# Kernel optimization log

Hardware: AMD Instinct MI355X
Metric: run time of the kernel (lower is better)

The kernel has to match this reference:

```python
import jax, jax.numpy as jnp
import numpy as np

NUM_CAPSULE = 16
DIM_CAPSULE = 64
ROUTINGS = 3
T_EPS = 1e-07


def squash(v, axis=-1):
    # NOTE: this repo's 'squash' is v / sqrt(||v||^2 + eps) (norm-only scaling)
    s = jnp.sum(v * v, axis=axis, keepdims=True)
    return v / jnp.sqrt(s + T_EPS)


def setup_inputs() -> dict:
    key = jax.random.key(0)
    k1, k2 = jax.random.split(key)
    B, N_in, D_in = 64, 512, 1024
    x = jax.random.normal(k1, (B, N_in, D_in), dtype=jnp.float32)
    # xavier-normal-ish init for W [1, D_in, num_capsule*dim_capsule]
    fan_in, fan_out = D_in, NUM_CAPSULE * DIM_CAPSULE
    std = float(np.sqrt(2.0 / (fan_in + fan_out)))
    W = jax.random.normal(k2, (1, D_in, NUM_CAPSULE * DIM_CAPSULE), dtype=jnp.float32) * std
    return {"x": x, "W": W}


def reference(x, W):
    B, N_in, D_in = x.shape
    # u_hat: [B, N_in, num_cap*dim_cap] -> [B, num_cap, N_in, dim_cap]
    u_hat = jnp.matmul(x, W[0])
    u_hat = u_hat.reshape(B, N_in, NUM_CAPSULE, DIM_CAPSULE).transpose(0, 2, 1, 3)
    b = jnp.zeros((B, NUM_CAPSULE, N_in), dtype=u_hat.dtype)
    outputs = None
    for i in range(ROUTINGS):
        # torch code permutes to [B, N_in, num_cap], softmaxes dim=2, permutes back:
        # equivalent to softmax over the num_capsule axis (axis=1)
        c = jax.nn.softmax(b, axis=1)  # [B, num_cap, N_in]
        outputs = squash(jnp.einsum('bij,bijk->bik', c, u_hat))  # [B, num_cap, dim_cap]
        if i < ROUTINGS - 1:
            b = jnp.einsum('bik,bijk->bij', outputs, u_hat)  # [B, num_cap, N_in]
    return outputs
```

## Files before the change

kernel.cpp:

```cpp
#include <hip/hip_runtime.h>
#include <stdint.h>

#define NUM_CAP 16
#define DIM_CAP 64
#define BATCH   64
#define N_IN    512
#define D_IN    1024
#define N_COL   1024
#define M_ROWS  (BATCH*N_IN)

typedef __attribute__((ext_vector_type(8))) short short8;
typedef __attribute__((ext_vector_type(4))) float f32x4;

__device__ __forceinline__ float bf2f(unsigned int u) {
  return __uint_as_float(u << 16);
}
__device__ __forceinline__ unsigned short f2bf_rne(float f) {
  unsigned int x = __float_as_uint(f);
  x += 0x7fffu + ((x >> 16) & 1u);
  return (unsigned short)(x >> 16);
}
__device__ __forceinline__ unsigned int pack_rne(unsigned int lo, unsigned int hi) {
  const unsigned int lr = lo + (0x7fffu + ((lo >> 16) & 1u));
  const unsigned int hr = hi + (0x7fffu + ((hi >> 16) & 1u));
  return (lr >> 16) | (hr & 0xffff0000u);
}

__global__ __launch_bounds__(256) void prep(
    const float* __restrict__ x, const float* __restrict__ W,
    unsigned short* __restrict__ xb, unsigned short* __restrict__ Wt) {
  const int t = threadIdx.x;
  if (blockIdx.x < 16384) {
    const size_t i = ((size_t)blockIdx.x * 256 + t) * 8;
    const uint4 a = *(const uint4*)(x + i);
    const uint4 b = *(const uint4*)(x + i + 4);
    uint4 p;
    p.x = pack_rne(a.x, a.y); p.y = pack_rne(a.z, a.w);
    p.z = pack_rne(b.x, b.y); p.w = pack_rne(b.z, b.w);
    *(uint4*)(xb + i) = p;
  } else {
    __shared__ float tile[32][33];
    const int bid = blockIdx.x - 16384;
    const int bx = bid & 31, by = bid >> 5;
    const int tx = t & 31, ty0 = t >> 5;
    #pragma unroll
    for (int r = 0; r < 4; r++) {
      const int ty = ty0 + r * 8;
      tile[ty][tx] = W[(size_t)(by * 32 + ty) * N_COL + bx * 32 + tx];
    }
    __syncthreads();
    #pragma unroll
    for (int r = 0; r < 4; r++) {
      const int ty = ty0 + r * 8;
      Wt[(size_t)(bx * 32 + ty) * D_IN + by * 32 + tx] = f2bf_rne(tile[tx][ty]);
    }
  }
}

__global__ __launch_bounds__(256) void gemm_uhat(
    const unsigned short* __restrict__ A,
    const unsigned short* __restrict__ Bt,
    unsigned short* __restrict__ C) {
  __shared__ __align__(16) unsigned short lA[128 * 32];
  __shared__ __align__(16) unsigned short lB[128 * 32];

  const int t = threadIdx.x;
  const int wave = t >> 6, lane = t & 63;
  const int xcd = blockIdx.x & 7, local = blockIdx.x >> 3;
  const int mt = xcd * 32 + (local >> 3), nt = local & 7;
  const int m0 = mt * 128, n0 = nt * 128;
  const int wm = wave & 1, wn = wave >> 1;

  f32x4 acc[4][4] = {};

  const int srow = lane >> 2;
  const int schunk = ((lane & 3) ^ ((srow >> 1) & 3)) * 8;

  for (int kt = 0; kt < D_IN / 32; ++kt) {
    const int k0 = kt * 32;
    __syncthreads();
    #pragma unroll
    for (int s0 = 0; s0 < 2; ++s0) {
      const int s = wave + s0 * 4;
      const unsigned short* ga = A + (size_t)(m0 + s * 16 + srow) * D_IN + k0 + schunk;
      __builtin_amdgcn_global_load_lds(
          (const __attribute__((address_space(1))) void*)ga,
          (__attribute__((address_space(3))) void*)(lA + s * 512), 16, 0, 0);
      const unsigned short* gb = Bt + (size_t)(n0 + s * 16 + srow) * D_IN + k0 + schunk;
      __builtin_amdgcn_global_load_lds(
          (const __attribute__((address_space(1))) void*)gb,
          (__attribute__((address_space(3))) void*)(lB + s * 512), 16, 0, 0);
    }
    __syncthreads();

    short8 af[4], bfr[4];
    const int rsel = lane & 15;
    const int q = lane >> 4;
    const int koff = (q ^ ((rsel >> 1) & 3)) * 8;
    #pragma unroll
    for (int tm = 0; tm < 4; tm++)
      af[tm] = *(const short8*)&lA[(wm * 64 + tm * 16 + rsel) * 32 + koff];
    #pragma unroll
    for (int tn = 0; tn < 4; tn++)
      bfr[tn] = *(const short8*)&lB[(wn * 64 + tn * 16 + rsel) * 32 + koff];
    #pragma unroll
    for (int tm = 0; tm < 4; tm++)
      #pragma unroll
      for (int tn = 0; tn < 4; tn++)
        acc[tm][tn] = __builtin_amdgcn_mfma_f32_16x16x32_bf16(
            af[tm], bfr[tn], acc[tm][tn], 0, 0, 0);
  }

  const int lrow = (lane >> 4) * 4, lcol = lane & 15;
  #pragma unroll
  for (int tm = 0; tm < 4; tm++)
    #pragma unroll
    for (int tn = 0; tn < 4; tn++)
      #pragma unroll
      for (int r = 0; r < 4; r++) {
        const int row = m0 + wm * 64 + tm * 16 + lrow + r;
        const int col = n0 + wn * 64 + tn * 16 + lcol;
        C[(size_t)row * N_COL + col] = f2bf_rne(acc[tm][tn][r]);
      }
}

__global__ __launch_bounds__(256) void s1q(
    const unsigned short* __restrict__ uhat, float* __restrict__ S1q) {
  const int t = threadIdx.x;
  const int b = blockIdx.x >> 3, s = blockIdx.x & 7;
  const unsigned short* up =
      uhat + (size_t)(b * N_IN + s * 64) * N_COL + t * 4;
  float4 a = make_float4(0.f, 0.f, 0.f, 0.f);
  #pragma unroll 8
  for (int j = 0; j < 64; ++j, up += N_COL) {
    const uint2 d = *(const uint2*)up;
    a.x += bf2f(d.x & 0xffffu);
    a.y += __uint_as_float(d.x & 0xffff0000u);
    a.z += bf2f(d.y & 0xffffu);
    a.w += __uint_as_float(d.y & 0xffff0000u);
  }
  *(float4*)&S1q[(size_t)blockIdx.x * 1024 + t * 4] = a;
}

__global__ __launch_bounds__(256) void route_mid(
    const unsigned short* __restrict__ uhat,
    const float* __restrict__ Vin,
    float* __restrict__ Pout,
    const int nstrips) {
  __shared__ float sq[16 * 68];
  __shared__ float red[4][1024];
  const int t = threadIdx.x;
  const int w = t >> 6, lane = t & 63;
  const int b = blockIdx.x >> 4, jt4 = blockIdx.x & 15;
  const int jt = jt4 * 4 + w;
  const int i_l = lane >> 2, c4 = lane & 3;

  float4 v4 = make_float4(0.f, 0.f, 0.f, 0.f);
  for (int s = 0; s < nstrips; ++s) {
    const float4 ps = *(const float4*)&Vin[((size_t)b * nstrips + s) * 1024 + t * 4];
    v4.x += ps.x; v4.y += ps.y; v4.z += ps.z; v4.w += ps.w;
  }
  float ss = v4.x * v4.x + v4.y * v4.y + v4.z * v4.z + v4.w * v4.w;
  #pragma unroll
  for (int d = 1; d < 16; d <<= 1) ss += __shfl_xor(ss, d);
  const float inv = 1.f / sqrtf(ss + 1e-7f);
  const int oi = t >> 4, ok = (t & 15) * 4;
  *(float4*)&sq[oi * 68 + ok] =
      make_float4(v4.x * inv, v4.y * inv, v4.z * inv, v4.w * inv);
  __syncthreads();

  float pv[16];
  #pragma unroll
  for (int q = 0; q < 4; q++)
    *(float4*)&pv[q * 4] = *(const float4*)&sq[i_l * 68 + c4 * 16 + q * 4];

  float acc[16];
  #pragma unroll
  for (int q = 0; q < 16; q++) acc[q] = 0.f;

  const unsigned short* ub =
      uhat + (size_t)(b * N_IN + jt * 8) * N_COL + lane * 16;

  for (int jj = 0; jj < 8; ++jj, ub += N_COL) {
    const uint4 d0 = *(const uint4*)ub;
    const uint4 d1 = *(const uint4*)(ub + 8);
    float u[16];
    #define UNP(wd, o) { u[(o)] = bf2f((wd) & 0xffffu); u[(o)+1] = __uint_as_float((wd) & 0xffff0000u); }
    UNP(d0.x, 0) UNP(d0.y, 2) UNP(d0.z, 4) UNP(d0.w, 6)
    UNP(d1.x, 8) UNP(d1.y, 10) UNP(d1.z, 12) UNP(d1.w, 14)
    #undef UNP

    float dot = 0.f;
    #pragma unroll
    for (int q = 0; q < 16; q++) dot = fmaf(pv[q], u[q], dot);
    dot += __shfl_xor(dot, 1);
    dot += __shfl_xor(dot, 2);
    const float e = __expf(dot);
    float s = e;
    #pragma unroll
    for (int d = 4; d < 64; d <<= 1) s += __shfl_xor(s, d);
    const float c = e / s;
    #pragma unroll
    for (int q = 0; q < 16; q++) acc[q] = fmaf(c, u[q], acc[q]);
  }

  #pragma unroll
  for (int q = 0; q < 4; q++)
    *(float4*)&red[w][lane * 16 + q * 4] = make_float4(
        acc[q * 4 + 0], acc[q * 4 + 1], acc[q * 4 + 2], acc[q * 4 + 3]);
  __syncthreads();
  float4 s4 = make_float4(0.f, 0.f, 0.f, 0.f);
  #pragma unroll
  for (int ww = 0; ww < 4; ++ww) {
    const float4 r = *(const float4*)&red[ww][t * 4];
    s4.x += r.x; s4.y += r.y; s4.z += r.z; s4.w += r.w;
  }
  *(float4*)&Pout[(size_t)blockIdx.x * 1024 + t * 4] = s4;
}

__global__ __launch_bounds__(64) void route_last(
    const float* __restrict__ P, float* __restrict__ dst) {
  const int bi = blockIdx.x;
  const int k = threadIdx.x;
  const int b = bi >> 4, i = bi & 15;
  const float* p = P + (size_t)b * 16 * 1024 + i * 64 + k;
  float s = 0.f;
  #pragma unroll
  for (int tt = 0; tt < 16; ++tt) s += p[(size_t)tt * 1024];
  float ss = s * s;
  #pragma unroll
  for (int d = 1; d < 64; d <<= 1) ss += __shfl_xor(ss, d);
  dst[bi * 64 + k] = s / sqrtf(ss + 1e-7f);
}

extern "C" void kernel_launch(void* const* d_in, const int* in_sizes, int n_in,
                              void* d_out, int out_size, void* d_ws, size_t ws_size,
                              hipStream_t stream) {
  const float* x = (const float*)d_in[0];
  const float* W = (const float*)d_in[1];
  float* out = (float*)d_out;

  char* ws = (char*)d_ws;
  unsigned short* Wt   = (unsigned short*)ws;
  unsigned short* uhat = (unsigned short*)(ws + (size_t)(2 << 20));
  unsigned short* xb   = (unsigned short*)(ws + (size_t)66 * (1 << 20));
  float* S1 = (float*)(ws + (size_t)130 * (1 << 20));
  float* P1 = (float*)(ws + (size_t)66 * (1 << 20));
  float* P2 = (float*)(ws + (size_t)71 * (1 << 20));

  prep<<<16384 + 1024, 256, 0, stream>>>(x, W, xb, Wt);
  gemm_uhat<<<2048, 256, 0, stream>>>(xb, Wt, uhat);
  s1q<<<512, 256, 0, stream>>>(uhat, S1);
  route_mid<<<1024, 256, 0, stream>>>(uhat, S1, P1, 8);
  route_mid<<<1024, 256, 0, stream>>>(uhat, P1, P2, 16);
  route_last<<<1024, 64, 0, stream>>>(P2, out);
}
```

Measured before the change: 322.5 us.

## Fuse x bf16 conversion and first routing sum into the u_hat GEMM

Drops the separate x-to-bf16 pass: the GEMM now loads fp32 x tiles straight into LDS and truncates to bf16 while building MFMA fragments. It also computes per-tile column sums of u_hat in the GEMM epilogue, which replaces the s1q kernel that re-read all of u_hat. The aim is to avoid one full write and read of x and one extra read of u_hat. In exchange, A-tile global and LDS traffic doubles because it is fp32, rounding changes from round-to-nearest-even to truncation, the first routing sum is taken from fp32 accumulators rather than stored bf16 values, and one route_mid loop is now unrolled.

```diff
diff --git a/kernel.cpp b/kernel.cpp
--- a/kernel.cpp
+++ b/kernel.cpp
@@ -20,49 +20,37 @@
   x += 0x7fffu + ((x >> 16) & 1u);
   return (unsigned short)(x >> 16);
 }
-__device__ __forceinline__ unsigned int pack_rne(unsigned int lo, unsigned int hi) {
-  const unsigned int lr = lo + (0x7fffu + ((lo >> 16) & 1u));
-  const unsigned int hr = hi + (0x7fffu + ((hi >> 16) & 1u));
-  return (lr >> 16) | (hr & 0xffff0000u);
-}
-
-__global__ __launch_bounds__(256) void prep(
-    const float* __restrict__ x, const float* __restrict__ W,
-    unsigned short* __restrict__ xb, unsigned short* __restrict__ Wt) {
+__device__ __forceinline__ unsigned int pack_trunc(unsigned int lo, unsigned int hi) {
+  return (lo >> 16) | (hi & 0xffff0000u);
+}
+
+__global__ __launch_bounds__(256) void prep_w(
+    const float* __restrict__ W, unsigned short* __restrict__ Wt) {
+  __shared__ float tile[32][33];
   const int t = threadIdx.x;
-  if (blockIdx.x < 16384) {
-    const size_t i = ((size_t)blockIdx.x * 256 + t) * 8;
-    const uint4 a = *(const uint4*)(x + i);
-    const uint4 b = *(const uint4*)(x + i + 4);
-    uint4 p;
-    p.x = pack_rne(a.x, a.y); p.y = pack_rne(a.z, a.w);
-    p.z = pack_rne(b.x, b.y); p.w = pack_rne(b.z, b.w);
-    *(uint4*)(xb + i) = p;
-  } else {
-    __shared__ float tile[32][33];
-    const int bid = blockIdx.x - 16384;
-    const int bx = bid & 31, by = bid >> 5;
-    const int tx = t & 31, ty0 = t >> 5;
-    #pragma unroll
-    for (int r = 0; r < 4; r++) {
-      const int ty = ty0 + r * 8;
-      tile[ty][tx] = W[(size_t)(by * 32 + ty) * N_COL + bx * 32 + tx];
-    }
-    __syncthreads();
-    #pragma unroll
-    for (int r = 0; r < 4; r++) {
-      const int ty = ty0 + r * 8;
-      Wt[(size_t)(bx * 32 + ty) * D_IN + by * 32 + tx] = f2bf_rne(tile[tx][ty]);
-    }
+  const int bx = blockIdx.x & 31, by = blockIdx.x >> 5;
+  const int tx = t & 31, ty0 = t >> 5;
+  #pragma unroll
+  for (int r = 0; r < 4; r++) {
+    const int ty = ty0 + r * 8;
+    tile[ty][tx] = W[(size_t)(by * 32 + ty) * N_COL + bx * 32 + tx];
+  }
+  __syncthreads();
+  #pragma unroll
+  for (int r = 0; r < 4; r++) {
+    const int ty = ty0 + r * 8;
+    Wt[(size_t)(bx * 32 + ty) * D_IN + by * 32 + tx] = f2bf_rne(tile[tx][ty]);
   }
 }
 
 __global__ __launch_bounds__(256) void gemm_uhat(
-    const unsigned short* __restrict__ A,
+    const float* __restrict__ A,
     const unsigned short* __restrict__ Bt,
-    unsigned short* __restrict__ C) {
-  __shared__ __align__(16) unsigned short lA[128 * 32];
+    unsigned short* __restrict__ C,
+    float* __restrict__ Pp) {
+  __shared__ __align__(16) float lAf[128 * 32];
   __shared__ __align__(16) unsigned short lB[128 * 32];
+  __shared__ float cs2[2][128];
 
   const int t = threadIdx.x;
   const int wave = t >> 6, lane = t & 63;
@@ -73,6 +61,8 @@
 
   f32x4 acc[4][4] = {};
 
+  const int arow_in_seg = lane >> 3;
+  const int achunk = lane & 7;
   const int srow = lane >> 2;
   const int schunk = ((lane & 3) ^ ((srow >> 1) & 3)) * 8;
 
@@ -80,12 +70,18 @@
     const int k0 = kt * 32;
     __syncthreads();
     #pragma unroll
+    for (int s0 = 0; s0 < 4; ++s0) {
+      const int s = wave + s0 * 4;
+      const int arow = s * 8 + arow_in_seg;
+      const int ac = (achunk ^ (arow & 7)) * 4;
+      const float* ga = A + (size_t)(m0 + arow) * D_IN + k0 + ac;
+      __builtin_amdgcn_global_load_lds(
+          (const __attribute__((address_space(1))) void*)ga,
+          (__attribute__((address_space(3))) void*)(lAf + s * 256), 16, 0, 0);
+    }
+    #pragma unroll
     for (int s0 = 0; s0 < 2; ++s0) {
       const int s = wave + s0 * 4;
-      const unsigned short* ga = A + (size_t)(m0 + s * 16 + srow) * D_IN + k0 + schunk;
-      __builtin_amdgcn_global_load_lds(
-          (const __attribute__((address_space(1))) void*)ga,
-          (__attribute__((address_space(3))) void*)(lA + s * 512), 16, 0, 0);
       const unsigned short* gb = Bt + (size_t)(n0 + s * 16 + srow) * D_IN + k0 + schunk;
       __builtin_amdgcn_global_load_lds(
           (const __attribute__((address_space(1))) void*)gb,
@@ -96,10 +92,20 @@
     short8 af[4], bfr[4];
     const int rsel = lane & 15;
     const int q = lane >> 4;
+    const int r7 = rsel & 7;
+    #pragma unroll
+    for (int tm = 0; tm < 4; tm++) {
+      const int row = wm * 64 + tm * 16 + rsel;
+      const f32x4 x0 = *(const f32x4*)&lAf[row * 32 + ((2 * q) ^ r7) * 4];
+      const f32x4 x1 = *(const f32x4*)&lAf[row * 32 + (((2 * q) | 1) ^ r7) * 4];
+      uint4 pk;
+      pk.x = pack_trunc(__float_as_uint(x0.x), __float_as_uint(x0.y));
+      pk.y = pack_trunc(__float_as_uint(x0.z), __float_as_uint(x0.w));
+      pk.z = pack_trunc(__float_as_uint(x1.x), __float_as_uint(x1.y));
+      pk.w = pack_trunc(__float_as_uint(x1.z), __float_as_uint(x1.w));
+      af[tm] = *(short8*)&pk;
+    }
     const int koff = (q ^ ((rsel >> 1) & 3)) * 8;
-    #pragma unroll
-    for (int tm = 0; tm < 4; tm++)
-      af[tm] = *(const short8*)&lA[(wm * 64 + tm * 16 + rsel) * 32 + koff];
     #pragma unroll
     for (int tn = 0; tn < 4; tn++)
       bfr[tn] = *(const short8*)&lB[(wn * 64 + tn * 16 + rsel) * 32 + koff];
@@ -122,24 +128,21 @@
         const int col = n0 + wn * 64 + tn * 16 + lcol;
         C[(size_t)row * N_COL + col] = f2bf_rne(acc[tm][tn][r]);
       }
-}
-
-__global__ __launch_bounds__(256) void s1q(
-    const unsigned short* __restrict__ uhat, float* __restrict__ S1q) {
-  const int t = threadIdx.x;
-  const int b = blockIdx.x >> 3, s = blockIdx.x & 7;
-  const unsigned short* up =
-      uhat + (size_t)(b * N_IN + s * 64) * N_COL + t * 4;
-  float4 a = make_float4(0.f, 0.f, 0.f, 0.f);
-  #pragma unroll 8
-  for (int j = 0; j < 64; ++j, up += N_COL) {
-    const uint2 d = *(const uint2*)up;
-    a.x += bf2f(d.x & 0xffffu);
-    a.y += __uint_as_float(d.x & 0xffff0000u);
-    a.z += bf2f(d.y & 0xffffu);
-    a.w += __uint_as_float(d.y & 0xffff0000u);
-  }
-  *(float4*)&S1q[(size_t)blockIdx.x * 1024 + t * 4] = a;
+
+  #pragma unroll
+  for (int tn = 0; tn < 4; tn++) {
+    float p = 0.f;
+    #pragma unroll
+    for (int tm = 0; tm < 4; tm++)
+      #pragma unroll
+      for (int r = 0; r < 4; r++) p += acc[tm][tn][r];
+    p += __shfl_xor(p, 16);
+    p += __shfl_xor(p, 32);
+    if (lane < 16) cs2[wm][wn * 64 + tn * 16 + lane] = p;
+  }
+  __syncthreads();
+  if (t < 128)
+    Pp[(size_t)mt * N_COL + n0 + t] = cs2[0][t] + cs2[1][t];
 }
 
 __global__ __launch_bounds__(256) void route_mid(
@@ -181,6 +184,7 @@
   const unsigned short* ub =
       uhat + (size_t)(b * N_IN + jt * 8) * N_COL + lane * 16;
 
+  #pragma unroll
   for (int jj = 0; jj < 8; ++jj, ub += N_COL) {
     const uint4 d0 = *(const uint4*)ub;
     const uint4 d1 = *(const uint4*)(ub + 8);
@@ -243,15 +247,13 @@
   char* ws = (char*)d_ws;
   unsigned short* Wt   = (unsigned short*)ws;
   unsigned short* uhat = (unsigned short*)(ws + (size_t)(2 << 20));
-  unsigned short* xb   = (unsigned short*)(ws + (size_t)66 * (1 << 20));
-  float* S1 = (float*)(ws + (size_t)130 * (1 << 20));
-  float* P1 = (float*)(ws + (size_t)66 * (1 << 20));
+  float* Pp = (float*)(ws + (size_t)66 * (1 << 20));
+  float* P1 = (float*)(ws + (size_t)67 * (1 << 20));
   float* P2 = (float*)(ws + (size_t)71 * (1 << 20));
 
-  prep<<<16384 + 1024, 256, 0, stream>>>(x, W, xb, Wt);
-  gemm_uhat<<<2048, 256, 0, stream>>>(xb, Wt, uhat);
-  s1q<<<512, 256, 0, stream>>>(uhat, S1);
-  route_mid<<<1024, 256, 0, stream>>>(uhat, S1, P1, 8);
+  prep_w<<<1024, 256, 0, stream>>>(W, Wt);
+  gemm_uhat<<<2048, 256, 0, stream>>>(x, Wt, uhat, Pp);
+  route_mid<<<1024, 256, 0, stream>>>(uhat, Pp, P1, 4);
   route_mid<<<1024, 256, 0, stream>>>(uhat, P1, P2, 16);
   route_last<<<1024, 64, 0, stream>>>(P2, out);
 }
```

New measurement: 383.9 us. +19.1%, slower.

## Fuse first routing column sums into GEMM epilogue and split squash into separate kernel

Applied to the files above, without the earlier changes.

The GEMM epilogue now reduces each 128x128 tile's accumulators over rows and writes per-tile column partial sums, which replaces the separate s1q pass that re-read all of u_hat. A small k_v kernel reduces the partials and applies the squash once per batch, so route_mid only loads a ready-made v. route_mid now runs on twice as many blocks with 4 rows per wave and software-prefetches the next row. The first-iteration sum is taken from fp32 accumulators rather than rounded bf16, and the extra launches add small overhead.

```diff
diff --git a/kernel.cpp b/kernel.cpp
--- a/kernel.cpp
+++ b/kernel.cpp
@@ -60,9 +60,11 @@
 __global__ __launch_bounds__(256) void gemm_uhat(
     const unsigned short* __restrict__ A,
     const unsigned short* __restrict__ Bt,
-    unsigned short* __restrict__ C) {
+    unsigned short* __restrict__ C,
+    float* __restrict__ Pp) {
   __shared__ __align__(16) unsigned short lA[128 * 32];
   __shared__ __align__(16) unsigned short lB[128 * 32];
+  __shared__ float cs2[2][128];
 
   const int t = threadIdx.x;
   const int wave = t >> 6, lane = t & 63;
@@ -122,51 +124,54 @@
         const int col = n0 + wn * 64 + tn * 16 + lcol;
         C[(size_t)row * N_COL + col] = f2bf_rne(acc[tm][tn][r]);
       }
-}
-
-__global__ __launch_bounds__(256) void s1q(
-    const unsigned short* __restrict__ uhat, float* __restrict__ S1q) {
-  const int t = threadIdx.x;
-  const int b = blockIdx.x >> 3, s = blockIdx.x & 7;
-  const unsigned short* up =
-      uhat + (size_t)(b * N_IN + s * 64) * N_COL + t * 4;
-  float4 a = make_float4(0.f, 0.f, 0.f, 0.f);
-  #pragma unroll 8
-  for (int j = 0; j < 64; ++j, up += N_COL) {
-    const uint2 d = *(const uint2*)up;
-    a.x += bf2f(d.x & 0xffffu);
-    a.y += __uint_as_float(d.x & 0xffff0000u);
-    a.z += bf2f(d.y & 0xffffu);
-    a.w += __uint_as_float(d.y & 0xffff0000u);
-  }
-  *(float4*)&S1q[(size_t)blockIdx.x * 1024 + t * 4] = a;
+
+  #pragma unroll
+  for (int tn = 0; tn < 4; tn++) {
+    float p = 0.f;
+    #pragma unroll
+    for (int tm = 0; tm < 4; tm++)
+      #pragma unroll
+      for (int r = 0; r < 4; r++) p += acc[tm][tn][r];
+    p += __shfl_xor(p, 16);
+    p += __shfl_xor(p, 32);
+    if (lane < 16) cs2[wm][wn * 64 + tn * 16 + lane] = p;
+  }
+  __syncthreads();
+  if (t < 128)
+    Pp[(size_t)mt * N_COL + n0 + t] = cs2[0][t] + cs2[1][t];
+}
+
+__global__ __launch_bounds__(256) void k_v(
+    const float* __restrict__ Pin, float* __restrict__ vout, const int nstrips) {
+  const int b = blockIdx.x, t = threadIdx.x;
+  float4 s = make_float4(0.f, 0.f, 0.f, 0.f);
+  for (int q = 0; q < nstrips; ++q) {
+    const float4 p = *(const float4*)&Pin[((size_t)b * nstrips + q) * 1024 + t * 4];
+    s.x += p.x; s.y += p.y; s.z += p.z; s.w += p.w;
+  }
+  float ss = s.x * s.x + s.y * s.y + s.z * s.z + s.w * s.w;
+  #pragma unroll
+  for (int d = 1; d < 16; d <<= 1) ss += __shfl_xor(ss, d);
+  const float inv = 1.f / sqrtf(ss + 1e-7f);
+  *(float4*)&vout[(size_t)b * 1024 + t * 4] =
+      make_float4(s.x * inv, s.y * inv, s.z * inv, s.w * inv);
 }
 
 __global__ __launch_bounds__(256) void route_mid(
     const unsigned short* __restrict__ uhat,
-    const float* __restrict__ Vin,
-    float* __restrict__ Pout,
-    const int nstrips) {
+    const float* __restrict__ v,
+    float* __restrict__ Pout) {
   __shared__ float sq[16 * 68];
   __shared__ float red[4][1024];
   const int t = threadIdx.x;
   const int w = t >> 6, lane = t & 63;
-  const int b = blockIdx.x >> 4, jt4 = blockIdx.x & 15;
-  const int jt = jt4 * 4 + w;
+  const int b = blockIdx.x >> 5, jt = blockIdx.x & 31;
   const int i_l = lane >> 2, c4 = lane & 3;
 
-  float4 v4 = make_float4(0.f, 0.f, 0.f, 0.f);
-  for (int s = 0; s < nstrips; ++s) {
-    const float4 ps = *(const float4*)&Vin[((size_t)b * nstrips + s) * 1024 + t * 4];
-    v4.x += ps.x; v4.y += ps.y; v4.z += ps.z; v4.w += ps.w;
-  }
-  float ss = v4.x * v4.x + v4.y * v4.y + v4.z * v4.z + v4.w * v4.w;
-  #pragma unroll
-  for (int d = 1; d < 16; d <<= 1) ss += __shfl_xor(ss, d);
-  const float inv = 1.f / sqrtf(ss + 1e-7f);
-  const int oi = t >> 4, ok = (t & 15) * 4;
-  *(float4*)&sq[oi * 68 + ok] =
-      make_float4(v4.x * inv, v4.y * inv, v4.z * inv, v4.w * inv);
+  {
+    const float4 vv = *(const float4*)&v[(size_t)b * 1024 + t * 4];
+    *(float4*)&sq[(t >> 4) * 68 + (t & 15) * 4] = vv;
+  }
   __syncthreads();
 
   float pv[16];
@@ -179,15 +184,21 @@
   for (int q = 0; q < 16; q++) acc[q] = 0.f;
 
   const unsigned short* ub =
-      uhat + (size_t)(b * N_IN + jt * 8) * N_COL + lane * 16;
-
-  for (int jj = 0; jj < 8; ++jj, ub += N_COL) {
-    const uint4 d0 = *(const uint4*)ub;
-    const uint4 d1 = *(const uint4*)(ub + 8);
+      uhat + (size_t)(b * N_IN + jt * 16 + w * 4) * N_COL + lane * 16;
+
+  uint4 c0 = *(const uint4*)ub;
+  uint4 c1 = *(const uint4*)(ub + 8);
+  #pragma unroll
+  for (int jj = 0; jj < 4; ++jj) {
+    uint4 n0v = c0, n1v = c1;
+    if (jj < 3) {
+      n0v = *(const uint4*)(ub + N_COL);
+      n1v = *(const uint4*)(ub + N_COL + 8);
+    }
     float u[16];
     #define UNP(wd, o) { u[(o)] = bf2f((wd) & 0xffffu); u[(o)+1] = __uint_as_float((wd) & 0xffff0000u); }
-    UNP(d0.x, 0) UNP(d0.y, 2) UNP(d0.z, 4) UNP(d0.w, 6)
-    UNP(d1.x, 8) UNP(d1.y, 10) UNP(d1.z, 12) UNP(d1.w, 14)
+    UNP(c0.x, 0) UNP(c0.y, 2) UNP(c0.z, 4) UNP(c0.w, 6)
+    UNP(c1.x, 8) UNP(c1.y, 10) UNP(c1.z, 12) UNP(c1.w, 14)
     #undef UNP
 
     float dot = 0.f;
@@ -202,6 +213,8 @@
     const float c = e / s;
     #pragma unroll
     for (int q = 0; q < 16; q++) acc[q] = fmaf(c, u[q], acc[q]);
+
+    c0 = n0v; c1 = n1v; ub += N_COL;
   }
 
   #pragma unroll
@@ -216,21 +229,6 @@
     s4.x += r.x; s4.y += r.y; s4.z += r.z; s4.w += r.w;
   }
   *(float4*)&Pout[(size_t)blockIdx.x * 1024 + t * 4] = s4;
-}
-
-__global__ __launch_bounds__(64) void route_last(
-    const float* __restrict__ P, float* __restrict__ dst) {
-  const int bi = blockIdx.x;
-  const int k = threadIdx.x;
-  const int b = bi >> 4, i = bi & 15;
-  const float* p = P + (size_t)b * 16 * 1024 + i * 64 + k;
-  float s = 0.f;
-  #pragma unroll
-  for (int tt = 0; tt < 16; ++tt) s += p[(size_t)tt * 1024];
-  float ss = s * s;
-  #pragma unroll
-  for (int d = 1; d < 64; d <<= 1) ss += __shfl_xor(ss, d);
-  dst[bi * 64 + k] = s / sqrtf(ss + 1e-7f);
 }
 
 extern "C" void kernel_launch(void* const* d_in, const int* in_sizes, int n_in,
@@ -243,15 +241,18 @@
   char* ws = (char*)d_ws;
   unsigned short* Wt   = (unsigned short*)ws;
   unsigned short* uhat = (unsigned short*)(ws + (size_t)(2 << 20));
-  unsigned short* xb   = (unsigned short*)(ws + (size_t)66 * (1 << 20));
-  float* S1 = (float*)(ws + (size_t)130 * (1 << 20));
-  float* P1 = (float*)(ws + (size_t)66 * (1 << 20));
-  float* P2 = (float*)(ws + (size_t)71 * (1 << 20));
+  float* Pp = (float*)(ws + (size_t)66 * (1 << 20));
+  float* v1 = (float*)(ws + (size_t)67 * (1 << 20));
+  float* v2 = (float*)(ws + (size_t)67 * (1 << 20) + (512 << 10));
+  unsigned short* xb = (unsigned short*)(ws + (size_t)68 * (1 << 20));
+  float* P1 = (float*)(ws + (size_t)68 * (1 << 20));
+  float* P2 = (float*)(ws + (size_t)76 * (1 << 20));
 
   prep<<<16384 + 1024, 256, 0, stream>>>(x, W, xb, Wt);
-  gemm_uhat<<<2048, 256, 0, stream>>>(xb, Wt, uhat);
-  s1q<<<512, 256, 0, stream>>>(uhat, S1);
-  route_mid<<<1024, 256, 0, stream>>>(uhat, S1, P1, 8);
-  route_mid<<<1024, 256, 0, stream>>>(uhat, P1, P2, 16);
-  route_last<<<1024, 64, 0, stream>>>(P2, out);
-}
+  gemm_uhat<<<2048, 256, 0, stream>>>(xb, Wt, uhat, Pp);
+  k_v<<<64, 256, 0, stream>>>(Pp, v1, 4);
+  route_mid<<<2048, 256, 0, stream>>>(uhat, v1, P1);
+  k_v<<<64, 256, 0, stream>>>(P1, v2, 32);
+  route_mid<<<2048, 256, 0, stream>>>(uhat, v2, P2);
+  k_v<<<64, 256, 0, stream>>>(P2, out, 32);
+}
```

Result: slower. 335.9 us (+4.2%).
